# Performance work log

Hardware: AMD Instinct MI355X
Metric: run time of the kernel (lower is better)

## Reference

```python
import jax, jax.numpy as jnp
import numpy as np

B = 2_000_000
IN, HID = 5, 4


def setup_inputs() -> dict:
    key = jax.random.key(0)
    ks = jax.random.split(key, 16)
    f = lambda k, shp: (jax.random.normal(k, shp, dtype=jnp.float32) * 0.3)
    inp = {
        "xl": jax.random.normal(ks[0], (B, IN), dtype=jnp.float32),
        "yl": jax.random.normal(ks[1], (B, IN), dtype=jnp.float32),
        "xr": jax.random.normal(ks[2], (B, IN), dtype=jnp.float32),
        "yr": jax.random.normal(ks[3], (B, IN), dtype=jnp.float32),
        # 6 stacked branches, order: [lxl, lyl, lxr, lyr, rxl, ryl]
        "W1": f(ks[4], (6, HID, IN)),
        "b1": f(ks[5], (6, HID)),
        "W2": f(ks[6], (6, HID, HID)),
        "b2": f(ks[7], (6, HID)),
        # fc3 with 2 outputs, order: [lxl, lyl, rxl, ryl] (branch idx 0,1,4,5)
        "W3_2": f(ks[8], (4, 2, HID)),
        "b3_2": f(ks[9], (4, 2)),
        # fc3 with 1 output, order: [lxr, lyr] (branch idx 2,3)
        "W3_1": f(ks[10], (2, 1, HID)),
        "b3_1": f(ks[11], (2, 1)),
        # fc4, order: [xl, yl]
        "W4": f(ks[12], (2, 1, HID)),
        "b4": f(ks[13], (2, 1)),
    }
    return inp


def reference(xl, yl, xr, yr, W1, b1, W2, b2, W3_2, b3_2, W3_1, b3_1, W4, b4):
    # Stack the six branch inputs: [6, B, 5]. NOTE: fc_1lyr consumes yl (yr unused),
    # faithful to the original forward.
    X = jnp.stack([xl, yl, xr, yl, xl, yl], axis=0)
    h1 = jax.nn.sigmoid(jnp.einsum("kbi,khi->kbh", X, W1) + b1[:, None, :])
    h2 = jax.nn.sigmoid(jnp.einsum("kbh,kgh->kbg", h1, W2) + b2[:, None, :])
    # fc3 heads with 2 outputs: branches lxl(0), lyl(1), rxl(4), ryl(5)
    h2_2 = h2[jnp.array([0, 1, 4, 5])]                       # [4, B, 4]
    o2 = jnp.einsum("kbh,koh->kbo", h2_2, W3_2) + b3_2[:, None, :]  # [4, B, 2]
    # fc3 heads with 1 output: branches lxr(2), lyr(3)
    h2_1 = h2[jnp.array([2, 3])]                             # [2, B, 4]
    o1 = jnp.einsum("kbh,koh->kbo", h2_1, W3_1) + b3_1[:, None, :]  # [2, B, 1]
    # concat (per-sample dim, was dim=0 unbatched)
    out_xl = jnp.concatenate([o2[0], o2[2]], axis=-1)        # [B, 4]
    out_yl = jnp.concatenate([o2[1], o2[3]], axis=-1)        # [B, 4]
    fc4xl = out_xl @ W4[0].T + b4[0]                         # [B, 1]
    fc4yl = out_yl @ W4[1].T + b4[1]                         # [B, 1]
    out = jnp.concatenate([o1[0], o1[1], fc4xl, fc4yl], axis=-1)  # [B, 4]
    return out
```

## Files before the change

### kernel.cpp

```cpp
#include <hip/hip_runtime.h>

#define NTHREADS 256

typedef float f32x2 __attribute__((ext_vector_type(2)));

#if defined(__has_builtin)
#if __has_builtin(__builtin_amdgcn_exp2f)
#define EXP2F __builtin_amdgcn_exp2f
#else
#define EXP2F exp2f
#endif
#else
#define EXP2F exp2f
#endif

__device__ __forceinline__ float rfl(float x) {
    return __uint_as_float(__builtin_amdgcn_readfirstlane(__float_as_uint(x)));
}

__device__ __forceinline__ f32x2 bc2(float w) {
    f32x2 r; r.x = w; r.y = w; return r;
}
__device__ __forceinline__ f32x2 pfma(f32x2 a, f32x2 b, f32x2 c) {
    return __builtin_elementwise_fma(a, b, c);
}

__device__ __forceinline__ void sig4(f32x2 v[4]) {
    const f32x2 C   = bc2(-1.442695040888963f);
    const f32x2 ONE = bc2(1.0f);
    f32x2 d[4];
    #pragma unroll
    for (int h = 0; h < 4; h++) {
        f32x2 m = v[h] * C;
        f32x2 e; e.x = EXP2F(m.x); e.y = EXP2F(m.y);
        d[h] = e + ONE;
    }
    f32x2 p01 = d[0] * d[1];
    f32x2 p23 = d[2] * d[3];
    f32x2 P   = p01 * p23;
    f32x2 r;
    r.x = __builtin_amdgcn_rcpf(P.x);
    r.y = __builtin_amdgcn_rcpf(P.y);
    f32x2 r01 = r * p23;
    f32x2 r23 = r * p01;
    v[0] = r01 * d[1];
    v[1] = r01 * d[0];
    v[2] = r23 * d[3];
    v[3] = r23 * d[2];
}

__global__ __launch_bounds__(NTHREADS, 4)
void mlp6_fused_kernel(const float* __restrict__ xl,
                       const float* __restrict__ yl,
                       const float* __restrict__ xr,
                       const float* __restrict__ W1, const float* __restrict__ b1,
                       const float* __restrict__ W2, const float* __restrict__ b2,
                       const float* __restrict__ W3_2, const float* __restrict__ b3_2,
                       const float* __restrict__ W3_1, const float* __restrict__ b3_1,
                       const float* __restrict__ W4, const float* __restrict__ b4,
                       float* __restrict__ out, int B)
{
    const int nq = B >> 1;
    int gq = blockIdx.x * NTHREADS + threadIdx.x;
    if (gq >= nq) gq = nq - 1;

    f32x2 LA[5], LB[5], LC[5];
    {
        const f32x2* x2 = (const f32x2*)xl + (long long)gq * 5;
        const f32x2* y2 = (const f32x2*)yl + (long long)gq * 5;
        const f32x2* c2 = (const f32x2*)xr + (long long)gq * 5;
        #pragma unroll
        for (int q = 0; q < 5; q++) LA[q] = x2[q];
        #pragma unroll
        for (int q = 0; q < 5; q++) LB[q] = y2[q];
        #pragma unroll
        for (int q = 0; q < 5; q++) LC[q] = c2[q];
    }
    f32x2 xp[5], yp[5];
    xp[0].x = LA[0].x; xp[0].y = LA[2].y;
    xp[1].x = LA[0].y; xp[1].y = LA[3].x;
    xp[2].x = LA[1].x; xp[2].y = LA[3].y;
    xp[3].x = LA[1].y; xp[3].y = LA[4].x;
    xp[4].x = LA[2].x; xp[4].y = LA[4].y;
    yp[0].x = LB[0].x; yp[0].y = LB[2].y;
    yp[1].x = LB[0].y; yp[1].y = LB[3].x;
    yp[2].x = LB[1].x; yp[2].y = LB[3].y;
    yp[3].x = LB[1].y; yp[3].y = LB[4].x;
    yp[4].x = LB[2].x; yp[4].y = LB[4].y;

    float fw[6][4];
    #pragma unroll
    for (int h = 0; h < 4; h++) {
        fw[0][h] = rfl(fmaf(W4[1], W3_2[4 + h],  W4[0] * W3_2[h]));
        fw[1][h] = rfl(fmaf(W4[5], W3_2[12 + h], W4[4] * W3_2[8 + h]));
        fw[2][h] = rfl(W3_1[h]);
        fw[3][h] = rfl(W3_1[4 + h]);
        fw[4][h] = rfl(fmaf(W4[3], W3_2[20 + h], W4[2] * W3_2[16 + h]));
        fw[5][h] = rfl(fmaf(W4[7], W3_2[28 + h], W4[6] * W3_2[24 + h]));
    }
    float fb0 = rfl(b3_1[0]);
    float fb1 = rfl(b3_1[1]);
    float fb2 = rfl(W4[0]*b3_2[0] + W4[1]*b3_2[1] + W4[2]*b3_2[4] + W4[3]*b3_2[5] + b4[0]);
    float fb3 = rfl(W4[4]*b3_2[2] + W4[5]*b3_2[3] + W4[6]*b3_2[6] + W4[7]*b3_2[7] + b4[1]);

    f32x2 o0 = bc2(fb0), o1 = bc2(fb1), o2 = bc2(fb2), o3 = bc2(fb3);

    auto branch = [&](int k, const f32x2 (&in)[5], f32x2& oslot) {
        f32x2 h[4];
        #pragma unroll
        for (int hh = 0; hh < 4; hh++) {
            f32x2 acc = bc2(b1[k*4 + hh]);
            #pragma unroll
            for (int q = 0; q < 5; q++)
                acc = pfma(in[q], bc2(W1[k*20 + hh*5 + q]), acc);
            h[hh] = acc;
        }
        sig4(h);
        f32x2 c[4];
        #pragma unroll
        for (int g = 0; g < 4; g++) {
            f32x2 acc = bc2(b2[k*4 + g]);
            #pragma unroll
            for (int q = 0; q < 4; q++)
                acc = pfma(h[q], bc2(W2[k*16 + g*4 + q]), acc);
            c[g] = acc;
        }
        sig4(c);
        #pragma unroll
        for (int g = 0; g < 4; g++)
            oslot = pfma(c[g], bc2(fw[k][g]), oslot);
    };

    branch(0, xp, o2);
    branch(4, xp, o2);
    xp[0].x = LC[0].x; xp[0].y = LC[2].y;
    xp[1].x = LC[0].y; xp[1].y = LC[3].x;
    xp[2].x = LC[1].x; xp[2].y = LC[3].y;
    xp[3].x = LC[1].y; xp[3].y = LC[4].x;
    xp[4].x = LC[2].x; xp[4].y = LC[4].y;
    branch(1, yp, o3);
    branch(3, yp, o1);
    branch(5, yp, o3);
    branch(2, xp, o0);

    float4 r0, r1;
    r0.x = o0.x; r0.y = o1.x; r0.z = o2.x; r0.w = o3.x;
    r1.x = o0.y; r1.y = o1.y; r1.z = o2.y; r1.w = o3.y;
    float4* out4 = (float4*)out;
    out4[(long long)gq * 2]     = r0;
    out4[(long long)gq * 2 + 1] = r1;
}

extern "C" void kernel_launch(void* const* d_in, const int* in_sizes, int n_in,
                              void* d_out, int out_size, void* d_ws, size_t ws_size,
                              hipStream_t stream) {
    const float* xl   = (const float*)d_in[0];
    const float* yl   = (const float*)d_in[1];
    const float* xr   = (const float*)d_in[2];
    const float* W1   = (const float*)d_in[4];
    const float* b1   = (const float*)d_in[5];
    const float* W2   = (const float*)d_in[6];
    const float* b2   = (const float*)d_in[7];
    const float* W3_2 = (const float*)d_in[8];
    const float* b3_2 = (const float*)d_in[9];
    const float* W3_1 = (const float*)d_in[10];
    const float* b3_1 = (const float*)d_in[11];
    const float* W4   = (const float*)d_in[12];
    const float* b4   = (const float*)d_in[13];
    float* out = (float*)d_out;

    int B = in_sizes[0] / 5;
    int nq = B >> 1;
    int blocks = (nq + NTHREADS - 1) / NTHREADS;
    mlp6_fused_kernel<<<blocks, NTHREADS, 0, stream>>>(
        xl, yl, xr, W1, b1, W2, b2, W3_2, b3_2, W3_1, b3_1, W4, b4, out, B);
}
```

Before: 39.47 us.

## Stage inputs through shared memory with coalesced float4 loads

Each block cooperatively loads its slice of xl, yl and xr into LDS using fully coalesced float4 reads, then each thread reads its two samples from LDS. This replaces per-thread strided float2 global loads and the manual deinterleaving shuffles. Block size changes to 320 threads, and a scalar tail kernel is added for batch sizes not divisible by the block's sample count. It adds a barrier and LDS traffic, with possible bank conflicts from the stride-10 reads.

```diff
diff --git a/kernel.cpp b/kernel.cpp
--- a/kernel.cpp
+++ b/kernel.cpp
@@ -1,6 +1,10 @@
 #include <hip/hip_runtime.h>
 
-#define NTHREADS 256
+#define NT 320
+#define NPAIR NT
+#define NSAMP (NT * 2)
+#define NFLT (NSAMP * 5)
+#define NF4 (NFLT / 4)
 
 typedef float f32x2 __attribute__((ext_vector_type(2)));
 
@@ -17,7 +21,6 @@
 __device__ __forceinline__ float rfl(float x) {
     return __uint_as_float(__builtin_amdgcn_readfirstlane(__float_as_uint(x)));
 }
-
 __device__ __forceinline__ f32x2 bc2(float w) {
     f32x2 r; r.x = w; r.y = w; return r;
 }
@@ -49,44 +52,38 @@
     v[3] = r23 * d[2];
 }
 
-__global__ __launch_bounds__(NTHREADS, 4)
-void mlp6_fused_kernel(const float* __restrict__ xl,
-                       const float* __restrict__ yl,
-                       const float* __restrict__ xr,
-                       const float* __restrict__ W1, const float* __restrict__ b1,
-                       const float* __restrict__ W2, const float* __restrict__ b2,
-                       const float* __restrict__ W3_2, const float* __restrict__ b3_2,
-                       const float* __restrict__ W3_1, const float* __restrict__ b3_1,
-                       const float* __restrict__ W4, const float* __restrict__ b4,
-                       float* __restrict__ out, int B)
+__global__ __launch_bounds__(NT, 4)
+void mlp6_main(const float* __restrict__ xl,
+               const float* __restrict__ yl,
+               const float* __restrict__ xr,
+               const float* __restrict__ W1, const float* __restrict__ b1,
+               const float* __restrict__ W2, const float* __restrict__ b2,
+               const float* __restrict__ W3_2, const float* __restrict__ b3_2,
+               const float* __restrict__ W3_1, const float* __restrict__ b3_1,
+               const float* __restrict__ W4, const float* __restrict__ b4,
+               float* __restrict__ out)
 {
-    const int nq = B >> 1;
-    int gq = blockIdx.x * NTHREADS + threadIdx.x;
-    if (gq >= nq) gq = nq - 1;
-
-    f32x2 LA[5], LB[5], LC[5];
+    __shared__ __align__(16) float sx[NFLT];
+    __shared__ __align__(16) float sy[NFLT];
+    __shared__ __align__(16) float sc[NFLT];
+
+    const int tid = threadIdx.x;
+    const int bid = blockIdx.x;
+
     {
-        const f32x2* x2 = (const f32x2*)xl + (long long)gq * 5;
-        const f32x2* y2 = (const f32x2*)yl + (long long)gq * 5;
-        const f32x2* c2 = (const f32x2*)xr + (long long)gq * 5;
-        #pragma unroll
-        for (int q = 0; q < 5; q++) LA[q] = x2[q];
-        #pragma unroll
-        for (int q = 0; q < 5; q++) LB[q] = y2[q];
-        #pragma unroll
-        for (int q = 0; q < 5; q++) LC[q] = c2[q];
-    }
-    f32x2 xp[5], yp[5];
-    xp[0].x = LA[0].x; xp[0].y = LA[2].y;
-    xp[1].x = LA[0].y; xp[1].y = LA[3].x;
-    xp[2].x = LA[1].x; xp[2].y = LA[3].y;
-    xp[3].x = LA[1].y; xp[3].y = LA[4].x;
-    xp[4].x = LA[2].x; xp[4].y = LA[4].y;
-    yp[0].x = LB[0].x; yp[0].y = LB[2].y;
-    yp[1].x = LB[0].y; yp[1].y = LB[3].x;
-    yp[2].x = LB[1].x; yp[2].y = LB[3].y;
-    yp[3].x = LB[1].y; yp[3].y = LB[4].x;
-    yp[4].x = LB[2].x; yp[4].y = LB[4].y;
+        const float4* gx = (const float4*)xl + (long long)bid * NF4;
+        const float4* gy = (const float4*)yl + (long long)bid * NF4;
+        const float4* gc = (const float4*)xr + (long long)bid * NF4;
+        float4* s4x = (float4*)sx;
+        float4* s4y = (float4*)sy;
+        float4* s4c = (float4*)sc;
+        #pragma unroll
+        for (int i = tid; i < NF4; i += NT) {
+            s4x[i] = gx[i];
+            s4y[i] = gy[i];
+            s4c[i] = gc[i];
+        }
+    }
 
     float fw[6][4];
     #pragma unroll
@@ -103,6 +100,18 @@
     float fb2 = rfl(W4[0]*b3_2[0] + W4[1]*b3_2[1] + W4[2]*b3_2[4] + W4[3]*b3_2[5] + b4[0]);
     float fb3 = rfl(W4[4]*b3_2[2] + W4[5]*b3_2[3] + W4[6]*b3_2[6] + W4[7]*b3_2[7] + b4[1]);
 
+    __syncthreads();
+
+    const float* bx = sx + 10 * tid;
+    const float* by = sy + 10 * tid;
+    const float* bc_ = sc + 10 * tid;
+    f32x2 xp[5], yp[5];
+    #pragma unroll
+    for (int q = 0; q < 5; q++) {
+        xp[q].x = bx[q]; xp[q].y = bx[5 + q];
+        yp[q].x = by[q]; yp[q].y = by[5 + q];
+    }
+
     f32x2 o0 = bc2(fb0), o1 = bc2(fb1), o2 = bc2(fb2), o3 = bc2(fb3);
 
     auto branch = [&](int k, const f32x2 (&in)[5], f32x2& oslot) {
@@ -133,11 +142,8 @@
 
     branch(0, xp, o2);
     branch(4, xp, o2);
-    xp[0].x = LC[0].x; xp[0].y = LC[2].y;
-    xp[1].x = LC[0].y; xp[1].y = LC[3].x;
-    xp[2].x = LC[1].x; xp[2].y = LC[3].y;
-    xp[3].x = LC[1].y; xp[3].y = LC[4].x;
-    xp[4].x = LC[2].x; xp[4].y = LC[4].y;
+    #pragma unroll
+    for (int q = 0; q < 5; q++) { xp[q].x = bc_[q]; xp[q].y = bc_[5 + q]; }
     branch(1, yp, o3);
     branch(3, yp, o1);
     branch(5, yp, o3);
@@ -146,9 +152,67 @@
     float4 r0, r1;
     r0.x = o0.x; r0.y = o1.x; r0.z = o2.x; r0.w = o3.x;
     r1.x = o0.y; r1.y = o1.y; r1.z = o2.y; r1.w = o3.y;
+    long long gq = (long long)bid * NPAIR + tid;
     float4* out4 = (float4*)out;
-    out4[(long long)gq * 2]     = r0;
-    out4[(long long)gq * 2 + 1] = r1;
+    out4[gq * 2]     = r0;
+    out4[gq * 2 + 1] = r1;
+}
+
+__global__ void mlp6_tail(const float* __restrict__ xl,
+                          const float* __restrict__ yl,
+                          const float* __restrict__ xr,
+                          const float* __restrict__ W1, const float* __restrict__ b1,
+                          const float* __restrict__ W2, const float* __restrict__ b2,
+                          const float* __restrict__ W3_2, const float* __restrict__ b3_2,
+                          const float* __restrict__ W3_1, const float* __restrict__ b3_1,
+                          const float* __restrict__ W4, const float* __restrict__ b4,
+                          float* __restrict__ out, int start, int B)
+{
+    int i = start + blockIdx.x * 64 + threadIdx.x;
+    if (i >= B) return;
+    const int p = i * 5;
+    float xa[5], ya[5], ca[5];
+    for (int q = 0; q < 5; q++) { xa[q]=xl[p+q]; ya[q]=yl[p+q]; ca[q]=xr[p+q]; }
+
+    float fw[6][4];
+    for (int h = 0; h < 4; h++) {
+        fw[0][h] = fmaf(W4[1], W3_2[4 + h],  W4[0] * W3_2[h]);
+        fw[1][h] = fmaf(W4[5], W3_2[12 + h], W4[4] * W3_2[8 + h]);
+        fw[2][h] = W3_1[h];
+        fw[3][h] = W3_1[4 + h];
+        fw[4][h] = fmaf(W4[3], W3_2[20 + h], W4[2] * W3_2[16 + h]);
+        fw[5][h] = fmaf(W4[7], W3_2[28 + h], W4[6] * W3_2[24 + h]);
+    }
+    float o[4];
+    o[0] = b3_1[0];
+    o[1] = b3_1[1];
+    o[2] = W4[0]*b3_2[0] + W4[1]*b3_2[1] + W4[2]*b3_2[4] + W4[3]*b3_2[5] + b4[0];
+    o[3] = W4[4]*b3_2[2] + W4[5]*b3_2[3] + W4[6]*b3_2[6] + W4[7]*b3_2[7] + b4[1];
+
+    auto branch = [&](int k, const float* xb) -> float {
+        float a[4], c[4];
+        for (int h = 0; h < 4; h++) {
+            float s = b1[k*4 + h];
+            for (int q = 0; q < 5; q++) s = fmaf(xb[q], W1[k*20 + h*5 + q], s);
+            a[h] = 1.0f / (1.0f + expf(-s));
+        }
+        for (int g = 0; g < 4; g++) {
+            float s = b2[k*4 + g];
+            for (int h = 0; h < 4; h++) s = fmaf(a[h], W2[k*16 + g*4 + h], s);
+            c[g] = 1.0f / (1.0f + expf(-s));
+        }
+        float r = 0.f;
+        for (int g = 0; g < 4; g++) r = fmaf(c[g], fw[k][g], r);
+        return r;
+    };
+    o[2] += branch(0, xa);
+    o[3] += branch(1, ya);
+    o[0] += branch(2, ca);
+    o[1] += branch(3, ya);
+    o[2] += branch(4, xa);
+    o[3] += branch(5, ya);
+    float4 r; r.x = o[0]; r.y = o[1]; r.z = o[2]; r.w = o[3];
+    ((float4*)out)[i] = r;
 }
 
 extern "C" void kernel_launch(void* const* d_in, const int* in_sizes, int n_in,
@@ -170,8 +234,13 @@
     float* out = (float*)d_out;
 
     int B = in_sizes[0] / 5;
-    int nq = B >> 1;
-    int blocks = (nq + NTHREADS - 1) / NTHREADS;
-    mlp6_fused_kernel<<<blocks, NTHREADS, 0, stream>>>(
-        xl, yl, xr, W1, b1, W2, b2, W3_2, b3_2, W3_1, b3_1, W4, b4, out, B);
-}
+    int nfull = B / NSAMP;
+    int rem   = B - nfull * NSAMP;
+    if (nfull > 0)
+        mlp6_main<<<nfull, NT, 0, stream>>>(
+            xl, yl, xr, W1, b1, W2, b2, W3_2, b3_2, W3_1, b3_1, W4, b4, out);
+    if (rem > 0)
+        mlp6_tail<<<(rem + 63) / 64, 64, 0, stream>>>(
+            xl, yl, xr, W1, b1, W2, b2, W3_2, b3_2, W3_1, b3_1, W4, b4, out,
+            nfull * NSAMP, B);
+}
```

Measured after the change: 49.79 us. +26.1%, slower.

## Split six-branch MLP across two block roles via grid y-dimension

Applied to the files above, without the earlier changes.

Launches twice as many blocks, each taking one of two roles. One role handles the xl and xr branches, the other handles the three yl branches. Each block reads fewer inputs and holds less register state, and the goal is more parallelism and occupancy for this compute-heavy kernel. In exchange, output writes become strided scalar stores interleaved between the two roles instead of full float4 stores, and weight-derived constants are recomputed per role.

```diff
diff --git a/kernel.cpp b/kernel.cpp
--- a/kernel.cpp
+++ b/kernel.cpp
@@ -1,6 +1,6 @@
 #include <hip/hip_runtime.h>
 
-#define NTHREADS 256
+#define NT 256
 
 typedef float f32x2 __attribute__((ext_vector_type(2)));
 
@@ -17,7 +17,6 @@
 __device__ __forceinline__ float rfl(float x) {
     return __uint_as_float(__builtin_amdgcn_readfirstlane(__float_as_uint(x)));
 }
-
 __device__ __forceinline__ f32x2 bc2(float w) {
     f32x2 r; r.x = w; r.y = w; return r;
 }
@@ -49,106 +48,140 @@
     v[3] = r23 * d[2];
 }
 
-__global__ __launch_bounds__(NTHREADS, 4)
-void mlp6_fused_kernel(const float* __restrict__ xl,
-                       const float* __restrict__ yl,
-                       const float* __restrict__ xr,
-                       const float* __restrict__ W1, const float* __restrict__ b1,
-                       const float* __restrict__ W2, const float* __restrict__ b2,
-                       const float* __restrict__ W3_2, const float* __restrict__ b3_2,
-                       const float* __restrict__ W3_1, const float* __restrict__ b3_1,
-                       const float* __restrict__ W4, const float* __restrict__ b4,
-                       float* __restrict__ out, int B)
+__global__ __launch_bounds__(NT, 4)
+void mlp6_split(const float* __restrict__ xl,
+                const float* __restrict__ yl,
+                const float* __restrict__ xr,
+                const float* __restrict__ W1, const float* __restrict__ b1,
+                const float* __restrict__ W2, const float* __restrict__ b2,
+                const float* __restrict__ W3_2, const float* __restrict__ b3_2,
+                const float* __restrict__ W3_1, const float* __restrict__ b3_1,
+                const float* __restrict__ W4, const float* __restrict__ b4,
+                float* __restrict__ out, int nq)
 {
-    const int nq = B >> 1;
-    int gq = blockIdx.x * NTHREADS + threadIdx.x;
+    int gq = blockIdx.x * NT + threadIdx.x;
     if (gq >= nq) gq = nq - 1;
-
-    f32x2 LA[5], LB[5], LC[5];
-    {
-        const f32x2* x2 = (const f32x2*)xl + (long long)gq * 5;
-        const f32x2* y2 = (const f32x2*)yl + (long long)gq * 5;
-        const f32x2* c2 = (const f32x2*)xr + (long long)gq * 5;
+    const int role = blockIdx.y;
+
+    if (role == 0) {
+        f32x2 xp[5], cp[5];
+        {
+            const f32x2* x2 = (const f32x2*)xl + (long long)gq * 5;
+            const f32x2* c2 = (const f32x2*)xr + (long long)gq * 5;
+            f32x2 LA[5], LC[5];
+            #pragma unroll
+            for (int q = 0; q < 5; q++) LA[q] = x2[q];
+            #pragma unroll
+            for (int q = 0; q < 5; q++) LC[q] = c2[q];
+            xp[0].x = LA[0].x; xp[0].y = LA[2].y;
+            xp[1].x = LA[0].y; xp[1].y = LA[3].x;
+            xp[2].x = LA[1].x; xp[2].y = LA[3].y;
+            xp[3].x = LA[1].y; xp[3].y = LA[4].x;
+            xp[4].x = LA[2].x; xp[4].y = LA[4].y;
+            cp[0].x = LC[0].x; cp[0].y = LC[2].y;
+            cp[1].x = LC[0].y; cp[1].y = LC[3].x;
+            cp[2].x = LC[1].x; cp[2].y = LC[3].y;
+            cp[3].x = LC[1].y; cp[3].y = LC[4].x;
+            cp[4].x = LC[2].x; cp[4].y = LC[4].y;
+        }
+        float fw0[4], fw4[4], fw2[4];
         #pragma unroll
-        for (int q = 0; q < 5; q++) LA[q] = x2[q];
+        for (int h = 0; h < 4; h++) {
+            fw0[h] = rfl(fmaf(W4[1], W3_2[4 + h],  W4[0] * W3_2[h]));
+            fw4[h] = rfl(fmaf(W4[3], W3_2[20 + h], W4[2] * W3_2[16 + h]));
+            fw2[h] = rfl(W3_1[h]);
+        }
+        float fb0 = rfl(b3_1[0]);
+        float fb2 = rfl(W4[0]*b3_2[0] + W4[1]*b3_2[1] + W4[2]*b3_2[4] + W4[3]*b3_2[5] + b4[0]);
+        f32x2 o0 = bc2(fb0), o2 = bc2(fb2);
+
+        auto br = [&](int k, const f32x2 (&in)[5], const float fwk[4], f32x2& oslot) {
+            f32x2 h[4];
+            #pragma unroll
+            for (int hh = 0; hh < 4; hh++) {
+                f32x2 acc = bc2(b1[k*4 + hh]);
+                #pragma unroll
+                for (int q = 0; q < 5; q++)
+                    acc = pfma(in[q], bc2(W1[k*20 + hh*5 + q]), acc);
+                h[hh] = acc;
+            }
+            sig4(h);
+            f32x2 c[4];
+            #pragma unroll
+            for (int g = 0; g < 4; g++) {
+                f32x2 acc = bc2(b2[k*4 + g]);
+                #pragma unroll
+                for (int q = 0; q < 4; q++)
+                    acc = pfma(h[q], bc2(W2[k*16 + g*4 + q]), acc);
+                c[g] = acc;
+            }
+            sig4(c);
+            #pragma unroll
+            for (int g = 0; g < 4; g++) oslot = pfma(c[g], bc2(fwk[g]), oslot);
+        };
+        br(0, xp, fw0, o2);
+        br(4, xp, fw4, o2);
+        br(2, cp, fw2, o0);
+
+        float* ob = out + (long long)gq * 8;
+        ob[0] = o0.x; ob[2] = o2.x;
+        ob[4] = o0.y; ob[6] = o2.y;
+    } else {
+        f32x2 yp[5];
+        {
+            const f32x2* y2 = (const f32x2*)yl + (long long)gq * 5;
+            f32x2 LB[5];
+            #pragma unroll
+            for (int q = 0; q < 5; q++) LB[q] = y2[q];
+            yp[0].x = LB[0].x; yp[0].y = LB[2].y;
+            yp[1].x = LB[0].y; yp[1].y = LB[3].x;
+            yp[2].x = LB[1].x; yp[2].y = LB[3].y;
+            yp[3].x = LB[1].y; yp[3].y = LB[4].x;
+            yp[4].x = LB[2].x; yp[4].y = LB[4].y;
+        }
+        float fw1[4], fw5[4], fw3[4];
         #pragma unroll
-        for (int q = 0; q < 5; q++) LB[q] = y2[q];
-        #pragma unroll
-        for (int q = 0; q < 5; q++) LC[q] = c2[q];
+        for (int h = 0; h < 4; h++) {
+            fw1[h] = rfl(fmaf(W4[5], W3_2[12 + h], W4[4] * W3_2[8 + h]));
+            fw5[h] = rfl(fmaf(W4[7], W3_2[28 + h], W4[6] * W3_2[24 + h]));
+            fw3[h] = rfl(W3_1[4 + h]);
+        }
+        float fb1 = rfl(b3_1[1]);
+        float fb3 = rfl(W4[4]*b3_2[2] + W4[5]*b3_2[3] + W4[6]*b3_2[6] + W4[7]*b3_2[7] + b4[1]);
+        f32x2 o1 = bc2(fb1), o3 = bc2(fb3);
+
+        auto br = [&](int k, const f32x2 (&in)[5], const float fwk[4], f32x2& oslot) {
+            f32x2 h[4];
+            #pragma unroll
+            for (int hh = 0; hh < 4; hh++) {
+                f32x2 acc = bc2(b1[k*4 + hh]);
+                #pragma unroll
+                for (int q = 0; q < 5; q++)
+                    acc = pfma(in[q], bc2(W1[k*20 + hh*5 + q]), acc);
+                h[hh] = acc;
+            }
+            sig4(h);
+            f32x2 c[4];
+            #pragma unroll
+            for (int g = 0; g < 4; g++) {
+                f32x2 acc = bc2(b2[k*4 + g]);
+                #pragma unroll
+                for (int q = 0; q < 4; q++)
+                    acc = pfma(h[q], bc2(W2[k*16 + g*4 + q]), acc);
+                c[g] = acc;
+            }
+            sig4(c);
+            #pragma unroll
+            for (int g = 0; g < 4; g++) oslot = pfma(c[g], bc2(fwk[g]), oslot);
+        };
+        br(1, yp, fw1, o3);
+        br(3, yp, fw3, o1);
+        br(5, yp, fw5, o3);
+
+        float* ob = out + (long long)gq * 8;
+        ob[1] = o1.x; ob[3] = o3.x;
+        ob[5] = o1.y; ob[7] = o3.y;
     }
-    f32x2 xp[5], yp[5];
-    xp[0].x = LA[0].x; xp[0].y = LA[2].y;
-    xp[1].x = LA[0].y; xp[1].y = LA[3].x;
-    xp[2].x = LA[1].x; xp[2].y = LA[3].y;
-    xp[3].x = LA[1].y; xp[3].y = LA[4].x;
-    xp[4].x = LA[2].x; xp[4].y = LA[4].y;
-    yp[0].x = LB[0].x; yp[0].y = LB[2].y;
-    yp[1].x = LB[0].y; yp[1].y = LB[3].x;
-    yp[2].x = LB[1].x; yp[2].y = LB[3].y;
-    yp[3].x = LB[1].y; yp[3].y = LB[4].x;
-    yp[4].x = LB[2].x; yp[4].y = LB[4].y;
-
-    float fw[6][4];
-    #pragma unroll
-    for (int h = 0; h < 4; h++) {
-        fw[0][h] = rfl(fmaf(W4[1], W3_2[4 + h],  W4[0] * W3_2[h]));
-        fw[1][h] = rfl(fmaf(W4[5], W3_2[12 + h], W4[4] * W3_2[8 + h]));
-        fw[2][h] = rfl(W3_1[h]);
-        fw[3][h] = rfl(W3_1[4 + h]);
-        fw[4][h] = rfl(fmaf(W4[3], W3_2[20 + h], W4[2] * W3_2[16 + h]));
-        fw[5][h] = rfl(fmaf(W4[7], W3_2[28 + h], W4[6] * W3_2[24 + h]));
-    }
-    float fb0 = rfl(b3_1[0]);
-    float fb1 = rfl(b3_1[1]);
-    float fb2 = rfl(W4[0]*b3_2[0] + W4[1]*b3_2[1] + W4[2]*b3_2[4] + W4[3]*b3_2[5] + b4[0]);
-    float fb3 = rfl(W4[4]*b3_2[2] + W4[5]*b3_2[3] + W4[6]*b3_2[6] + W4[7]*b3_2[7] + b4[1]);
-
-    f32x2 o0 = bc2(fb0), o1 = bc2(fb1), o2 = bc2(fb2), o3 = bc2(fb3);
-
-    auto branch = [&](int k, const f32x2 (&in)[5], f32x2& oslot) {
-        f32x2 h[4];
-        #pragma unroll
-        for (int hh = 0; hh < 4; hh++) {
-            f32x2 acc = bc2(b1[k*4 + hh]);
-            #pragma unroll
-            for (int q = 0; q < 5; q++)
-                acc = pfma(in[q], bc2(W1[k*20 + hh*5 + q]), acc);
-            h[hh] = acc;
-        }
-        sig4(h);
-        f32x2 c[4];
-        #pragma unroll
-        for (int g = 0; g < 4; g++) {
-            f32x2 acc = bc2(b2[k*4 + g]);
-            #pragma unroll
-            for (int q = 0; q < 4; q++)
-                acc = pfma(h[q], bc2(W2[k*16 + g*4 + q]), acc);
-            c[g] = acc;
-        }
-        sig4(c);
-        #pragma unroll
-        for (int g = 0; g < 4; g++)
-            oslot = pfma(c[g], bc2(fw[k][g]), oslot);
-    };
-
-    branch(0, xp, o2);
-    branch(4, xp, o2);
-    xp[0].x = LC[0].x; xp[0].y = LC[2].y;
-    xp[1].x = LC[0].y; xp[1].y = LC[3].x;
-    xp[2].x = LC[1].x; xp[2].y = LC[3].y;
-    xp[3].x = LC[1].y; xp[3].y = LC[4].x;
-    xp[4].x = LC[2].x; xp[4].y = LC[4].y;
-    branch(1, yp, o3);
-    branch(3, yp, o1);
-    branch(5, yp, o3);
-    branch(2, xp, o0);
-
-    float4 r0, r1;
-    r0.x = o0.x; r0.y = o1.x; r0.z = o2.x; r0.w = o3.x;
-    r1.x = o0.y; r1.y = o1.y; r1.z = o2.y; r1.w = o3.y;
-    float4* out4 = (float4*)out;
-    out4[(long long)gq * 2]     = r0;
-    out4[(long long)gq * 2 + 1] = r1;
 }
 
 extern "C" void kernel_launch(void* const* d_in, const int* in_sizes, int n_in,
@@ -169,9 +202,9 @@
     const float* b4   = (const float*)d_in[13];
     float* out = (float*)d_out;
 
-    int B = in_sizes[0] / 5;
+    int B  = in_sizes[0] / 5;
     int nq = B >> 1;
-    int blocks = (nq + NTHREADS - 1) / NTHREADS;
-    mlp6_fused_kernel<<<blocks, NTHREADS, 0, stream>>>(
-        xl, yl, xr, W1, b1, W2, b2, W3_2, b3_2, W3_1, b3_1, W4, b4, out, B);
-}
+    dim3 grid((nq + NT - 1) / NT, 2);
+    mlp6_split<<<grid, NT, 0, stream>>>(
+        xl, yl, xr, W1, b1, W2, b2, W3_2, b3_2, W3_1, b3_1, W4, b4, out, nq);
+}
```

Result: slower. 41.41 us (+4.9%).
